# Performance work log

Measured on AMD Instinct MI355X. Metric: run time of the kernel, lower is better.

Reference implementation:

```python
import jax, jax.numpy as jnp
import numpy as np

D_MODEL = 1024
N_HEADS = 16
DH = D_MODEL // N_HEADS
ROPE_THETA = 10000.0


def rotate_half(u):
    h = u.shape[-1] // 2
    return jnp.concatenate([-u[..., h:], u[..., :h]], axis=-1)


def apply_rope(q, k, cos, sin):
    return q * cos + rotate_half(q) * sin, k * cos + rotate_half(k) * sin


def setup_inputs() -> dict:
    key = jax.random.key(0)
    ks = jax.random.split(key, 6)
    B, S = 2, 2048
    x = jax.random.normal(ks[0], (B, S, D_MODEL), dtype=jnp.float32)
    y = jax.random.normal(ks[1], (B, S, D_MODEL), dtype=jnp.float32)
    wq = 0.01 * jax.random.normal(ks[2], (D_MODEL, D_MODEL), dtype=jnp.float32)
    wk = 0.01 * jax.random.normal(ks[3], (D_MODEL, D_MODEL), dtype=jnp.float32)
    wv = 0.01 * jax.random.normal(ks[4], (D_MODEL, D_MODEL), dtype=jnp.float32)
    wo = 0.01 * jax.random.normal(ks[5], (D_MODEL, D_MODEL), dtype=jnp.float32)
    return {"x": x, "y": y, "wq": wq, "wk": wk, "wv": wv, "wo": wo}


def reference(x, y, wq, wk, wv, wo):
    B, S, D = x.shape
    past_length = 0  # default; kv_cache=None

    Q = x @ wq.T                      # (B,S,D)
    K = y                             # NOTE: K is y un-projected (as in source)
    V = y @ wv.T
    # K1 = x @ wk.T is computed in the source but immediately overwritten
    # by the buggy second apply_rope call -> wk is unused in the output.
    V1 = x @ wo.T

    def heads(t):
        return t.reshape(B, S, N_HEADS, DH).transpose(0, 2, 1, 3)  # (B,H,S,dh)

    q_h, k_h, v_h, v1_h = heads(Q), heads(K), heads(V), heads(V1)

    # RoPE tables (past_length:past_length+S rows of the cache)
    freqs = 1.0 / ROPE_THETA ** (jnp.arange(0, DH, 2, dtype=jnp.float32) / DH)
    emb = jnp.arange(past_length, past_length + S, dtype=jnp.float32)[:, None] * freqs[None, :]
    cos = jnp.concatenate([jnp.cos(emb), jnp.cos(emb)], axis=-1)[None, None]  # (1,1,S,dh)
    sin = jnp.concatenate([jnp.sin(emb), jnp.sin(emb)], axis=-1)[None, None]

    q_h, k_h = apply_rope(q_h, k_h, cos, sin)
    # faithful to source: k1 = rope applied AGAIN to the already-roped k
    _, k1_h = apply_rope(q_h, k_h, cos, sin)

    k_full = jnp.concatenate([k_h, k1_h], axis=2)   # (B,H,2S,dh)
    v_full = jnp.concatenate([v_h, v1_h], axis=2)
    S_full = k_full.shape[2]

    # mask: tril(diagonal=past_length) over (S,S_full), last S cols = eye(S)
    rows = jnp.arange(S)[:, None]
    cols = jnp.arange(S_full)[None, :]
    mask = cols <= rows + past_length
    mask = mask.at[:, -S:].set(jnp.eye(S, dtype=bool))  # (S,S_full)

    scores = jnp.einsum("bhqd,bhkd->bhqk", q_h, k_full) / jnp.sqrt(jnp.asarray(DH, x.dtype))
    scores = jnp.where(mask[None, None], scores, jnp.asarray(-1e30, x.dtype))
    attn = jax.nn.softmax(scores, axis=-1)
    out = jnp.einsum("bhqk,bhkd->bhqd", attn, v_full)
    out = out.transpose(0, 2, 1, 3).reshape(B, S, D)

    k_ret = k_full[:, :, :-S, :]
    return out, k_ret
```

## Files before the change

### kernel.cpp

```cpp
#include <hip/hip_runtime.h>

#define DM 1024
#define NHEADS 16
#define DHEAD 64
#define BB 2
#define SS 2048
#define BH (BB*NHEADS)

typedef __attribute__((ext_vector_type(8))) short short8;
typedef __attribute__((ext_vector_type(4))) float float4v;
typedef unsigned short ushort_t;

#define LN1E4_D32 0.28782313662425572f
#define SM_SCALE  0.18033688011112042f

static __device__ __forceinline__ unsigned short f2bf(float f) {
    union { float f; unsigned u; } v; v.f = f;
    unsigned r = v.u + 0x7fffu + ((v.u >> 16) & 1u);
    return (unsigned short)(r >> 16);
}
static __device__ __forceinline__ float bf2f(unsigned short u) {
    union { float f; unsigned u; } v; v.u = ((unsigned)u) << 16;
    return v.f;
}
static __device__ __forceinline__ unsigned cvtpk_bf16(float lo, float hi) {
    unsigned r;
    asm("v_cvt_pk_bf16_f32 %0, %1, %2" : "=v"(r) : "v"(lo), "v"(hi));
    return r;
}
static __device__ __forceinline__ float ex2(float x) {
    float r;
    asm("v_exp_f32 %0, %1" : "=v"(r) : "v"(x));
    return r;
}

static __device__ __forceinline__ void gload16(const ushort_t* g, ushort_t* l) {
    __builtin_amdgcn_global_load_lds(
        (const __attribute__((address_space(1))) void*)g,
        (__attribute__((address_space(3))) void*)l, 16, 0, 0);
}

__global__ __launch_bounds__(256) void prep_kernel(
        const float* __restrict__ x, const float* __restrict__ y,
        const float* __restrict__ wq, const float* __restrict__ wv,
        const float* __restrict__ wo,
        ushort_t* __restrict__ xb, ushort_t* __restrict__ wqb,
        ushort_t* __restrict__ wvb, ushort_t* __restrict__ wob,
        float* __restrict__ kout, ushort_t* __restrict__ khb,
        ushort_t* __restrict__ yb) {
    if (blockIdx.x < 3584) {
        int C = blockIdx.x * 256 + threadIdx.x;
        int c  = C & 511;
        int tl = C >> 9;
        int rb = tl >> 5, kb = tl & 31;
        const float* src; ushort_t* dst; int r0;
        if (rb < 32)      { src = x;  r0 = rb * 128;        dst = xb  + (size_t)tl * 4096; }
        else if (rb < 40) { src = wq; r0 = (rb - 32) * 128; dst = wqb + (size_t)(((rb - 32) * 32) + kb) * 4096; }
        else if (rb < 48) { src = wv; r0 = (rb - 40) * 128; dst = wvb + (size_t)(((rb - 40) * 32) + kb) * 4096; }
        else              { src = wo; r0 = (rb - 48) * 128; dst = wob + (size_t)(((rb - 48) * 32) + kb) * 4096; }
        int row = c >> 2, g = c & 3;
        int kk3 = g ^ ((row >> 1) & 3);
        const float* s = src + (size_t)(r0 + row) * DM + kb * 32 + kk3 * 8;
        float4 a0 = *reinterpret_cast<const float4*>(s);
        float4 a1 = *reinterpret_cast<const float4*>(s + 4);
        short8 v;
        v[0] = (short)f2bf(a0.x); v[1] = (short)f2bf(a0.y);
        v[2] = (short)f2bf(a0.z); v[3] = (short)f2bf(a0.w);
        v[4] = (short)f2bf(a1.x); v[5] = (short)f2bf(a1.y);
        v[6] = (short)f2bf(a1.z); v[7] = (short)f2bf(a1.w);
        *reinterpret_cast<short8*>(dst + c * 8) = v;
        return;
    }
    int t = (blockIdx.x - 3584) * 256 + threadIdx.x;
    int i8 = t & 3;
    int s  = (t >> 2) & (SS - 1);
    int bh = t >> 13;
    int h = bh & (NHEADS - 1), b = bh >> 4;

    const float* yp = y + ((size_t)(b * SS + s)) * DM + h * DHEAD + i8 * 8;
    float4 a0 = *reinterpret_cast<const float4*>(yp);
    float4 a1 = *reinterpret_cast<const float4*>(yp + 4);
    float4 b0 = *reinterpret_cast<const float4*>(yp + 32);
    float4 b1 = *reinterpret_cast<const float4*>(yp + 36);
    float u0[8] = {a0.x, a0.y, a0.z, a0.w, a1.x, a1.y, a1.z, a1.w};
    float u1[8] = {b0.x, b0.y, b0.z, b0.w, b1.x, b1.y, b1.z, b1.w};
    float lo[8], hi[8];
#pragma unroll
    for (int j = 0; j < 8; j++) {
        int i = i8 * 8 + j;
        float freq = __expf(-(float)i * LN1E4_D32);
        float th = (float)s * freq;
        float cv, sv;
        __sincosf(th, &sv, &cv);
        lo[j] = u0[j] * cv - u1[j] * sv;
        hi[j] = u1[j] * cv + u0[j] * sv;
    }
    float* op = kout + ((size_t)bh * SS + s) * DHEAD + i8 * 8;
    *reinterpret_cast<float4*>(op)      = (float4){lo[0], lo[1], lo[2], lo[3]};
    *reinterpret_cast<float4*>(op + 4)  = (float4){lo[4], lo[5], lo[6], lo[7]};
    *reinterpret_cast<float4*>(op + 32) = (float4){hi[0], hi[1], hi[2], hi[3]};
    *reinterpret_cast<float4*>(op + 36) = (float4){hi[4], hi[5], hi[6], hi[7]};

    ushort_t* kb = khb + ((size_t)bh * 32 + (s >> 6)) * 4096 + (s & 63) * 64;
    short8 vlo, vhi;
#pragma unroll
    for (int j = 0; j < 8; j++) { vlo[j] = (short)f2bf(lo[j]); vhi[j] = (short)f2bf(hi[j]); }
    *reinterpret_cast<short8*>(kb + ((i8 ^ (s & 7)) << 3))       = vlo;
    *reinterpret_cast<short8*>(kb + (((i8 + 4) ^ (s & 7)) << 3)) = vhi;

    int rowm = b * SS + s;
    int rowin = rowm & 127, rbm = rowm >> 7;
    int g = i8 ^ ((rowin >> 1) & 3);
    ushort_t* yt = yb + ((size_t)(rbm * 32 + h * 2)) * 4096 + rowin * 32 + (g << 3);
    short8 ulo, uhi;
#pragma unroll
    for (int j = 0; j < 8; j++) { ulo[j] = (short)f2bf(u0[j]); uhi[j] = (short)f2bf(u1[j]); }
    *reinterpret_cast<short8*>(yt)        = ulo;
    *reinterpret_cast<short8*>(yt + 4096) = uhi;
}

__global__ __launch_bounds__(256, 2) void gemm3_kernel(
        const ushort_t* __restrict__ xb, const ushort_t* __restrict__ yb,
        const ushort_t* __restrict__ wqb, const ushort_t* __restrict__ wvb,
        const ushort_t* __restrict__ wob,
        ushort_t* __restrict__ qh, ushort_t* __restrict__ vt, ushort_t* __restrict__ v1h) {
    __shared__ __align__(16) char smem[49152];
    ushort_t* As = (ushort_t*)smem;
    ushort_t* Bs = (ushort_t*)(smem + 16384);
    ushort_t* Cs = (ushort_t*)(smem + 32768);
    ushort_t (*Ct)[136] = (ushort_t(*)[136])smem;

    int bid = blockIdx.x;
    int xcd = bid & 7;
    int s_  = bid >> 3;
    int merged = (s_ < 32);
    int t_  = s_ & 31;
    int n0  = (t_ >> 2) * 128;
    int m0  = (xcd * 4 + (t_ & 3)) * 128;

    const ushort_t* A  = merged ? xb : yb;
    const ushort_t* W1 = merged ? wqb : wvb;

    const ushort_t* Atl = A   + (size_t)(m0 >> 7) * 32 * 4096;
    const ushort_t* W1t = W1  + (size_t)(n0 >> 7) * 32 * 4096;
    const ushort_t* W2t = wob + (size_t)(n0 >> 7) * 32 * 4096;

    int tid = threadIdx.x;
    int wave = tid >> 6, lane = tid & 63, quad = lane >> 4, l15 = lane & 15;
    int wr = (wave >> 1) * 64, wc = (wave & 1) * 64;

    int gi0 = tid * 8, gi1 = (256 + tid) * 8;
    int li0 = (tid & 192) * 8, li1 = (256 + (tid & 192)) * 8;

    int aoff[4], boff[4];
#pragma unroll
    for (int mi = 0; mi < 4; mi++) {
        int row = wr + mi * 16 + l15;
        aoff[mi] = row * 32 + ((quad ^ ((row >> 1) & 3)) << 3);
    }
#pragma unroll
    for (int ni = 0; ni < 4; ni++) {
        int row = wc + ni * 16 + l15;
        boff[ni] = row * 32 + ((quad ^ ((row >> 1) & 3)) << 3);
    }

    float4v acc1[4][4], acc2[4][4];
#pragma unroll
    for (int a = 0; a < 4; a++)
#pragma unroll
        for (int b = 0; b < 4; b++) {
            acc1[a][b] = (float4v){0.f, 0.f, 0.f, 0.f};
            acc2[a][b] = (float4v){0.f, 0.f, 0.f, 0.f};
        }

    gload16(Atl + gi0, As + li0); gload16(Atl + gi1, As + li1);
    gload16(W1t + gi0, Bs + li0); gload16(W1t + gi1, Bs + li1);
    if (merged) { gload16(W2t + gi0, Cs + li0); gload16(W2t + gi1, Cs + li1); }
    int cur = 0;

    for (int kb = 0; kb < 32; kb++) {
        __syncthreads();
        if (kb + 1 < 32) {
            const ushort_t* at = Atl + (size_t)(kb + 1) * 4096;
            const ushort_t* w1 = W1t + (size_t)(kb + 1) * 4096;
            int nb = (cur ^ 1) * 4096;
            gload16(at + gi0, As + nb + li0); gload16(at + gi1, As + nb + li1);
            gload16(w1 + gi0, Bs + nb + li0); gload16(w1 + gi1, Bs + nb + li1);
            if (merged) {
                const ushort_t* w2 = W2t + (size_t)(kb + 1) * 4096;
                gload16(w2 + gi0, Cs + nb + li0); gload16(w2 + gi1, Cs + nb + li1);
            }
        }
        const ushort_t* Ac = As + cur * 4096;
        const ushort_t* Bc = Bs + cur * 4096;
        const ushort_t* Cc = Cs + cur * 4096;
        short8 af[4], b1[4];
#pragma unroll
        for (int mi = 0; mi < 4; mi++)
            af[mi] = *reinterpret_cast<const short8*>(&Ac[aoff[mi]]);
#pragma unroll
        for (int ni = 0; ni < 4; ni++)
            b1[ni] = *reinterpret_cast<const short8*>(&Bc[boff[ni]]);
#pragma unroll
        for (int mi = 0; mi < 4; mi++)
#pragma unroll
            for (int ni = 0; ni < 4; ni++)
                acc1[mi][ni] = __builtin_amdgcn_mfma_f32_16x16x32_bf16(af[mi], b1[ni], acc1[mi][ni], 0, 0, 0);
        if (merged) {
            short8 b2[4];
#pragma unroll
            for (int ni = 0; ni < 4; ni++)
                b2[ni] = *reinterpret_cast<const short8*>(&Cc[boff[ni]]);
#pragma unroll
            for (int mi = 0; mi < 4; mi++)
#pragma unroll
                for (int ni = 0; ni < 4; ni++)
                    acc2[mi][ni] = __builtin_amdgcn_mfma_f32_16x16x32_bf16(af[mi], b2[ni], acc2[mi][ni], 0, 0, 0);
        }
        cur ^= 1;
    }

    int h0 = n0 >> 6;
    if (merged) {
#pragma unroll
        for (int mi = 0; mi < 4; mi++)
#pragma unroll
            for (int r = 0; r < 4; r++) {
                int m = m0 + wr + mi * 16 + quad * 4 + r;
                float pos = (float)(m & (SS - 1));
#pragma unroll
                for (int ni = 0; ni < 2; ni++) {
                    int d = ni * 16 + l15;
                    float f = __expf(-(float)d * LN1E4_D32);
                    float th = pos * f;
                    float cv, sv;
                    __sincosf(th, &sv, &cv);
                    cv *= SM_SCALE; sv *= SM_SCALE;
                    float u0 = acc1[mi][ni][r], u1 = acc1[mi][ni + 2][r];
                    acc1[mi][ni][r]     = u0 * cv - u1 * sv;
                    acc1[mi][ni + 2][r] = u1 * cv + u0 * sv;
                }
            }
        __syncthreads();
#pragma unroll
        for (int mi = 0; mi < 4; mi++)
#pragma unroll
            for (int ni = 0; ni < 4; ni++) {
                int col = wc + ni * 16 + l15;
#pragma unroll
                for (int r = 0; r < 4; r++)
                    Ct[wr + mi * 16 + quad * 4 + r][col] = f2bf(acc1[mi][ni][r]);
            }
        __syncthreads();
#pragma unroll
        for (int it = 0; it < 8; it++) {
            int c = it * 256 + tid;
            int o = c >> 3, j = c & 7;
            int hh = o >> 7, mr = o & 127;
            int m = m0 + mr, b = m >> 11, si = m & (SS - 1);
            uint4 v = *reinterpret_cast<const uint4*>(&Ct[mr][hh * 64 + j * 8]);
            *reinterpret_cast<uint4*>(
                &qh[((size_t)((b * NHEADS + h0 + hh) * SS + si)) * DHEAD + j * 8]) = v;
        }
        __syncthreads();
#pragma unroll
        for (int mi = 0; mi < 4; mi++)
#pragma unroll
            for (int ni = 0; ni < 4; ni++) {
                int col = wc + ni * 16 + l15;
#pragma unroll
                for (int r = 0; r < 4; r++)
                    Ct[wr + mi * 16 + quad * 4 + r][col] = f2bf(acc2[mi][ni][r]);
            }
        __syncthreads();
#pragma unroll
        for (int it = 0; it < 8; it++) {
            int c = it * 256 + tid;
            int o = c >> 3, j = c & 7;
            int hh = o >> 7, mr = o & 127;
            int m = m0 + mr, b = m >> 11, si = m & (SS - 1);
            uint4 v = *reinterpret_cast<const uint4*>(&Ct[mr][hh * 64 + j * 8]);
            *reinterpret_cast<uint4*>(
                &v1h[((size_t)((b * NHEADS + h0 + hh) * SS + si)) * DHEAD + j * 8]) = v;
        }
    } else {
        __syncthreads();
#pragma unroll
        for (int mi = 0; mi < 4; mi++)
#pragma unroll
            for (int ni = 0; ni < 4; ni++) {
                int col = wc + ni * 16 + l15;
#pragma unroll
                for (int r = 0; r < 4; r++)
                    Ct[wr + mi * 16 + quad * 4 + r][col] = f2bf(acc1[mi][ni][r]);
            }
        __syncthreads();
        int b = m0 >> 11;
        int s0 = m0 & (SS - 1);
#pragma unroll
        for (int it = 0; it < 8; it++) {
            int c = it * 256 + tid;
            int dh  = c & 63;
            int k16 = (c >> 6) & 15;
            int hh  = c >> 10;
            short8 v;
#pragma unroll
            for (int e = 0; e < 8; e++)
                v[e] = (short)Ct[k16 * 8 + e][hh * 64 + dh];
            int kt = (s0 >> 6) + (k16 >> 3);
            size_t off = ((size_t)((b * NHEADS + h0 + hh) * 32 + kt)) * 4096
                       + dh * 64 + (((k16 & 7) ^ (dh & 7)) << 3);
            *reinterpret_cast<short8*>(&vt[off]) = v;
        }
    }
}

template<bool MASKED>
static __device__ __forceinline__ void attn_tile(
        const ushort_t* __restrict__ Kc, const ushort_t* __restrict__ Vc, int kbase,
        int quad, int l15, int q0w, const short8* qf, const short8& onesf,
        ushort_t* __restrict__ Psw, float4v* Oa, float4v& sum4) {
    float4v sa[4];
#pragma unroll
    for (int t2 = 0; t2 < 4; t2++) sa[t2] = (float4v){0.f, 0.f, 0.f, 0.f};
    __builtin_amdgcn_s_setprio(1);
#pragma unroll
    for (int t2 = 0; t2 < 4; t2++) {
        int key = t2 * 16 + l15;
        int ro = key * 64, sw = key & 7;
#pragma unroll
        for (int half = 0; half < 2; half++) {
            short8 kf = *reinterpret_cast<const short8*>(&Kc[ro + (((half * 4 + quad) ^ sw) << 3)]);
            sa[t2] = __builtin_amdgcn_mfma_f32_16x16x32_bf16(kf, qf[half], sa[t2], 0, 0, 0);
        }
    }
    __builtin_amdgcn_s_setprio(0);
    int query = q0w + l15;
    int swl = l15 & 7;
#pragma unroll
    for (int t2 = 0; t2 < 4; t2++) {
        float p[4];
#pragma unroll
        for (int r = 0; r < 4; r++) {
            float e = ex2(sa[t2][r]);
            if (MASKED) {
                int key = kbase + t2 * 16 + quad * 4 + r;
                p[r] = (key <= query) ? e : 0.f;
            } else {
                p[r] = e;
            }
        }
        unsigned w0 = cvtpk_bf16(p[0], p[1]);
        unsigned w1 = cvtpk_bf16(p[2], p[3]);
        int chunk = (((t2 * 2 + (quad >> 1)) ^ swl) << 3) + (quad & 1) * 4;
        *reinterpret_cast<unsigned*>(&Psw[l15 * 64 + chunk])     = w0;
        *reinterpret_cast<unsigned*>(&Psw[l15 * 64 + chunk + 2]) = w1;
    }
    short8 pf0 = *reinterpret_cast<const short8*>(&Psw[l15 * 64 + ((quad ^ swl) << 3)]);
    short8 pf1 = *reinterpret_cast<const short8*>(&Psw[l15 * 64 + (((4 + quad) ^ swl) << 3)]);
    __builtin_amdgcn_s_setprio(1);
#pragma unroll
    for (int t = 0; t < 4; t++) {
        int dh = t * 16 + l15;
        int ro = dh * 64, sw = dh & 7;
        short8 vf0 = *reinterpret_cast<const short8*>(&Vc[ro + ((quad ^ sw) << 3)]);
        short8 vf1 = *reinterpret_cast<const short8*>(&Vc[ro + (((4 + quad) ^ sw) << 3)]);
        Oa[t] = __builtin_amdgcn_mfma_f32_16x16x32_bf16(pf0, vf0, Oa[t], 0, 0, 0);
        Oa[t] = __builtin_amdgcn_mfma_f32_16x16x32_bf16(pf1, vf1, Oa[t], 0, 0, 0);
    }
    sum4 = __builtin_amdgcn_mfma_f32_16x16x32_bf16(pf0, onesf, sum4, 0, 0, 0);
    sum4 = __builtin_amdgcn_mfma_f32_16x16x32_bf16(pf1, onesf, sum4, 0, 0, 0);
    __builtin_amdgcn_s_setprio(0);
}

__global__ __launch_bounds__(512, 4) void attn_kernel(
        const ushort_t* __restrict__ qh, const float* __restrict__ kf32,
        const ushort_t* __restrict__ khb, const ushort_t* __restrict__ vtb,
        const ushort_t* __restrict__ v1h, float* __restrict__ out) {
    __shared__ __align__(16) ushort_t Ks[4][4096];
    __shared__ __align__(16) ushort_t Vt[4][4096];
    __shared__ __align__(16) ushort_t Ps[8][1024];

    int bid = blockIdx.x;
    int bh = (bid & 7) * 4 + ((bid >> 3) & 3);
    int p  = bid >> 5;

    int tid = threadIdx.x, wave = tid >> 6, lane = tid & 63, quad = lane >> 4, l15 = lane & 15;
    int jq  = (wave < 4) ? p : (31 - p);
    int q0w = jq * 64 + (wave & 3) * 16;
    const ushort_t* qp  = qh  + (size_t)bh * SS * DHEAD;
    const float*    kp  = kf32 + (size_t)bh * SS * DHEAD;
    const ushort_t* v1p = v1h + (size_t)bh * SS * DHEAD;
    const ushort_t* ktb = khb + (size_t)bh * 32 * 4096;
    const ushort_t* vtt = vtb + (size_t)bh * 32 * 4096;

    short8 qf[2];
    qf[0] = *reinterpret_cast<const short8*>(&qp[(q0w + l15) * DHEAD + quad * 8]);
    qf[1] = *reinterpret_cast<const short8*>(&qp[(q0w + l15) * DHEAD + 32 + quad * 8]);
    short8 onesf;
#pragma unroll
    for (int j = 0; j < 8; j++) onesf[j] = (short)0x3F80;

    float4v Oa[4];
#pragma unroll
    for (int t = 0; t < 4; t++) Oa[t] = (float4v){0.f, 0.f, 0.f, 0.f};
    float4v sum4 = (float4v){0.f, 0.f, 0.f, 0.f};

    int gi = tid * 8;
    int li = (tid & 448) * 8;

    int ntiles = 32 - p;
    gload16(ktb + gi, &Ks[0][li]);               gload16(vtt + gi, &Vt[0][li]);
    gload16(ktb + 4096 + gi, &Ks[1][li]);        gload16(vtt + 4096 + gi, &Vt[1][li]);

    int kt = 0;
    for (; kt + 1 < ntiles; kt += 2) {
        __syncthreads();
        if (kt + 2 < ntiles) {
            const ushort_t* gk = ktb + (size_t)(kt + 2) * 4096;
            const ushort_t* gv = vtt + (size_t)(kt + 2) * 4096;
            int nb = (kt + 2) & 3;
            gload16(gk + gi, &Ks[nb][li]);
            gload16(gv + gi, &Vt[nb][li]);
        }
        if (kt + 3 < ntiles) {
            const ushort_t* gk = ktb + (size_t)(kt + 3) * 4096;
            const ushort_t* gv = vtt + (size_t)(kt + 3) * 4096;
            int nb = (kt + 3) & 3;
            gload16(gk + gi, &Ks[nb][li]);
            gload16(gv + gi, &Vt[nb][li]);
        }
        {
            int kbase = kt * 64, sl = kt & 3;
            if (kbase <= q0w + 15) {
                if (kbase + 63 <= q0w)
                    attn_tile<false>(Ks[sl], Vt[sl], kbase, quad, l15, q0w, qf, onesf,
                                     &Ps[wave][0], Oa, sum4);
                else
                    attn_tile<true>(Ks[sl], Vt[sl], kbase, quad, l15, q0w, qf, onesf,
                                    &Ps[wave][0], Oa, sum4);
            }
        }
        {
            int kbase = (kt + 1) * 64, sl = (kt + 1) & 3;
            if (kbase <= q0w + 15) {
                if (kbase + 63 <= q0w)
                    attn_tile<false>(Ks[sl], Vt[sl], kbase, quad, l15, q0w, qf, onesf,
                                     &Ps[wave][0], Oa, sum4);
                else
                    attn_tile<true>(Ks[sl], Vt[sl], kbase, quad, l15, q0w, qf, onesf,
                                    &Ps[wave][0], Oa, sum4);
            }
        }
    }
    if (kt < ntiles) {
        __syncthreads();
        int kbase = kt * 64, sl = kt & 3;
        if (kbase <= q0w + 15) {
            if (kbase + 63 <= q0w)
                attn_tile<false>(Ks[sl], Vt[sl], kbase, quad, l15, q0w, qf, onesf,
                                 &Ps[wave][0], Oa, sum4);
            else
                attn_tile<true>(Ks[sl], Vt[sl], kbase, quad, l15, q0w, qf, onesf,
                                &Ps[wave][0], Oa, sum4);
        }
    }

    float* sdiag = reinterpret_cast<float*>(&Ps[wave][32]);

    {
        int sk = q0w + l15;
        const float* krow = kp + (size_t)sk * DHEAD;
        short8 k1lo, k1hi;
#pragma unroll
        for (int j = 0; j < 8; j++) {
            int d = quad * 8 + j;
            float f = __expf(-(float)d * LN1E4_D32);
            float th = (float)sk * f;
            float cv, sv;
            __sincosf(th, &sv, &cv);
            float a = krow[d], b2 = krow[d + 32];
            k1lo[j] = (short)f2bf(a * cv - b2 * sv);
            k1hi[j] = (short)f2bf(b2 * cv + a * sv);
        }
        float4v sd4 = (float4v){0.f, 0.f, 0.f, 0.f};
        sd4 = __builtin_amdgcn_mfma_f32_16x16x32_bf16(qf[0], k1lo, sd4, 0, 0, 0);
        sd4 = __builtin_amdgcn_mfma_f32_16x16x32_bf16(qf[1], k1hi, sd4, 0, 0, 0);
#pragma unroll
        for (int r = 0; r < 4; r++)
            if (l15 == quad * 4 + r) sdiag[l15] = sd4[r];

        int b = bh >> 4, h = bh & (NHEADS - 1);
#pragma unroll
        for (int r = 0; r < 4; r++) {
            float pd = ex2(sdiag[quad * 4 + r]);
            int query = q0w + quad * 4 + r;
            float linv = 1.f / (sum4[r] + pd);
#pragma unroll
            for (int t = 0; t < 4; t++) {
                float v1v = bf2f(v1p[query * DHEAD + t * 16 + l15]);
                float o = (Oa[t][r] + pd * v1v) * linv;
                out[(b * SS + query) * DM + h * DHEAD + t * 16 + l15] = o;
            }
        }
    }
}

extern "C" void kernel_launch(void* const* d_in, const int* in_sizes, int n_in,
                              void* d_out, int out_size, void* d_ws, size_t ws_size,
                              hipStream_t stream) {
    const float* x  = (const float*)d_in[0];
    const float* y  = (const float*)d_in[1];
    const float* wq = (const float*)d_in[2];
    const float* wv = (const float*)d_in[4];
    const float* wo = (const float*)d_in[5];
    float* outp  = (float*)d_out;
    float* k_out = outp + (size_t)BB * SS * DM;

    char* ws = (char*)d_ws;
    ushort_t* vtb = (ushort_t*)(ws);
    ushort_t* v1b = (ushort_t*)(ws + (8ull  << 20));
    ushort_t* qhb = (ushort_t*)(ws + (16ull << 20));
    ushort_t* khb = (ushort_t*)(ws + (24ull << 20));
    ushort_t* xb  = (ushort_t*)(ws + (32ull << 20));
    ushort_t* yb  = (ushort_t*)(ws + (40ull << 20));
    ushort_t* wqb = (ushort_t*)(ws + (48ull << 20));
    ushort_t* wvb = (ushort_t*)(ws + (50ull << 20));
    ushort_t* wob = (ushort_t*)(ws + (52ull << 20));

    prep_kernel<<<4608, 256, 0, stream>>>(x, y, wq, wv, wo, xb, wqb, wvb, wob,
                                          k_out, khb, yb);
    gemm3_kernel<<<512, 256, 0, stream>>>(xb, yb, wqb, wvb, wob, qhb, vtb, v1b);
    attn_kernel<<<512, 512, 0, stream>>>(qhb, k_out, khb, vtb, v1b, outp);
}
```

Measured before the change: 167.5 us.

## Keep softmax probabilities in registers via 16x16x16 MFMA and reorder V layout

Removes the per-wave LDS round trip for the P matrix. The score accumulator layout is fed directly as the A operand of 16x16x16 bf16 MFMAs. The V-transpose writer in the projection kernel is changed so each lane's 8-element V chunk matches the key ordering the register-resident P fragments use, and the row-sum now uses four small MFMAs against a ones vector. The cost is twice as many (smaller) MFMA instructions in exchange for dropping the LDS stores, loads and the Ps buffer.

```diff
diff --git a/kernel.cpp b/kernel.cpp
--- a/kernel.cpp
+++ b/kernel.cpp
@@ -8,6 +8,7 @@
 #define BH (BB*NHEADS)
 
 typedef __attribute__((ext_vector_type(8))) short short8;
+typedef __attribute__((ext_vector_type(4))) short short4v;
 typedef __attribute__((ext_vector_type(4))) float float4v;
 typedef unsigned short ushort_t;
 
@@ -32,6 +33,12 @@
     float r;
     asm("v_exp_f32 %0, %1" : "=v"(r) : "v"(x));
     return r;
+}
+static __device__ __forceinline__ short4v lo4(short8 v) {
+    return __builtin_shufflevector(v, v, 0, 1, 2, 3);
+}
+static __device__ __forceinline__ short4v hi4(short8 v) {
+    return __builtin_shufflevector(v, v, 4, 5, 6, 7);
 }
 
 static __device__ __forceinline__ void gload16(const ushort_t* g, ushort_t* l) {
@@ -300,16 +307,22 @@
 #pragma unroll
         for (int it = 0; it < 8; it++) {
             int c = it * 256 + tid;
-            int dh  = c & 63;
-            int k16 = (c >> 6) & 15;
-            int hh  = c >> 10;
+            int dh6 = c & 63;
+            int rest = c >> 6;
+            int hh = rest >> 4;
+            int th = (rest >> 3) & 1;
+            int cq = rest & 7;
+            int q = cq >> 1, sHalf = cq & 1;
             short8 v;
 #pragma unroll
-            for (int e = 0; e < 8; e++)
-                v[e] = (short)Ct[k16 * 8 + e][hh * 64 + dh];
-            int kt = (s0 >> 6) + (k16 >> 3);
+            for (int e = 0; e < 8; e++) {
+                int t2 = 2 * sHalf + (e >> 2), j = e & 3;
+                int kw = 16 * t2 + 4 * q + j;
+                v[e] = (short)Ct[th * 64 + kw][hh * 64 + dh6];
+            }
+            int kt = (s0 >> 6) + th;
             size_t off = ((size_t)((b * NHEADS + h0 + hh) * 32 + kt)) * 4096
-                       + dh * 64 + (((k16 & 7) ^ (dh & 7)) << 3);
+                       + dh6 * 64 + ((cq ^ (dh6 & 7)) << 3);
             *reinterpret_cast<short8*>(&vt[off]) = v;
         }
     }
@@ -318,8 +331,8 @@
 template<bool MASKED>
 static __device__ __forceinline__ void attn_tile(
         const ushort_t* __restrict__ Kc, const ushort_t* __restrict__ Vc, int kbase,
-        int quad, int l15, int q0w, const short8* qf, const short8& onesf,
-        ushort_t* __restrict__ Psw, float4v* Oa, float4v& sum4) {
+        int quad, int l15, int q0w, const short8* qf, const short4v& ones4,
+        float4v* Oa, float4v& sum4) {
     float4v sa[4];
 #pragma unroll
     for (int t2 = 0; t2 < 4; t2++) sa[t2] = (float4v){0.f, 0.f, 0.f, 0.f};
@@ -336,7 +349,7 @@
     }
     __builtin_amdgcn_s_setprio(0);
     int query = q0w + l15;
-    int swl = l15 & 7;
+    short4v pa[4];
 #pragma unroll
     for (int t2 = 0; t2 < 4; t2++) {
         float p[4];
@@ -350,26 +363,26 @@
                 p[r] = e;
             }
         }
-        unsigned w0 = cvtpk_bf16(p[0], p[1]);
-        unsigned w1 = cvtpk_bf16(p[2], p[3]);
-        int chunk = (((t2 * 2 + (quad >> 1)) ^ swl) << 3) + (quad & 1) * 4;
-        *reinterpret_cast<unsigned*>(&Psw[l15 * 64 + chunk])     = w0;
-        *reinterpret_cast<unsigned*>(&Psw[l15 * 64 + chunk + 2]) = w1;
-    }
-    short8 pf0 = *reinterpret_cast<const short8*>(&Psw[l15 * 64 + ((quad ^ swl) << 3)]);
-    short8 pf1 = *reinterpret_cast<const short8*>(&Psw[l15 * 64 + (((4 + quad) ^ swl) << 3)]);
+        union { short4v s; unsigned u[2]; } pu;
+        pu.u[0] = cvtpk_bf16(p[0], p[1]);
+        pu.u[1] = cvtpk_bf16(p[2], p[3]);
+        pa[t2] = pu.s;
+    }
     __builtin_amdgcn_s_setprio(1);
+#pragma unroll
+    for (int t2 = 0; t2 < 4; t2++)
+        sum4 = __builtin_amdgcn_mfma_f32_16x16x16bf16_1k(pa[t2], ones4, sum4, 0, 0, 0);
 #pragma unroll
     for (int t = 0; t < 4; t++) {
         int dh = t * 16 + l15;
         int ro = dh * 64, sw = dh & 7;
-        short8 vf0 = *reinterpret_cast<const short8*>(&Vc[ro + ((quad ^ sw) << 3)]);
-        short8 vf1 = *reinterpret_cast<const short8*>(&Vc[ro + (((4 + quad) ^ sw) << 3)]);
-        Oa[t] = __builtin_amdgcn_mfma_f32_16x16x32_bf16(pf0, vf0, Oa[t], 0, 0, 0);
-        Oa[t] = __builtin_amdgcn_mfma_f32_16x16x32_bf16(pf1, vf1, Oa[t], 0, 0, 0);
-    }
-    sum4 = __builtin_amdgcn_mfma_f32_16x16x32_bf16(pf0, onesf, sum4, 0, 0, 0);
-    sum4 = __builtin_amdgcn_mfma_f32_16x16x32_bf16(pf1, onesf, sum4, 0, 0, 0);
+        short8 v0 = *reinterpret_cast<const short8*>(&Vc[ro + (((quad * 2 + 0) ^ sw) << 3)]);
+        short8 v1 = *reinterpret_cast<const short8*>(&Vc[ro + (((quad * 2 + 1) ^ sw) << 3)]);
+        Oa[t] = __builtin_amdgcn_mfma_f32_16x16x16bf16_1k(pa[0], lo4(v0), Oa[t], 0, 0, 0);
+        Oa[t] = __builtin_amdgcn_mfma_f32_16x16x16bf16_1k(pa[1], hi4(v0), Oa[t], 0, 0, 0);
+        Oa[t] = __builtin_amdgcn_mfma_f32_16x16x16bf16_1k(pa[2], lo4(v1), Oa[t], 0, 0, 0);
+        Oa[t] = __builtin_amdgcn_mfma_f32_16x16x16bf16_1k(pa[3], hi4(v1), Oa[t], 0, 0, 0);
+    }
     __builtin_amdgcn_s_setprio(0);
 }
 
@@ -379,7 +392,7 @@
         const ushort_t* __restrict__ v1h, float* __restrict__ out) {
     __shared__ __align__(16) ushort_t Ks[4][4096];
     __shared__ __align__(16) ushort_t Vt[4][4096];
-    __shared__ __align__(16) ushort_t Ps[8][1024];
+    __shared__ float sdiag_s[8][16];
 
     int bid = blockIdx.x;
     int bh = (bid & 7) * 4 + ((bid >> 3) & 3);
@@ -397,9 +410,9 @@
     short8 qf[2];
     qf[0] = *reinterpret_cast<const short8*>(&qp[(q0w + l15) * DHEAD + quad * 8]);
     qf[1] = *reinterpret_cast<const short8*>(&qp[(q0w + l15) * DHEAD + 32 + quad * 8]);
-    short8 onesf;
-#pragma unroll
-    for (int j = 0; j < 8; j++) onesf[j] = (short)0x3F80;
+    short4v ones4;
+#pragma unroll
+    for (int j = 0; j < 4; j++) ones4[j] = (short)0x3F80;
 
     float4v Oa[4];
 #pragma unroll
@@ -434,22 +447,18 @@
             int kbase = kt * 64, sl = kt & 3;
             if (kbase <= q0w + 15) {
                 if (kbase + 63 <= q0w)
-                    attn_tile<false>(Ks[sl], Vt[sl], kbase, quad, l15, q0w, qf, onesf,
-                                     &Ps[wave][0], Oa, sum4);
+                    attn_tile<false>(Ks[sl], Vt[sl], kbase, quad, l15, q0w, qf, ones4, Oa, sum4);
                 else
-                    attn_tile<true>(Ks[sl], Vt[sl], kbase, quad, l15, q0w, qf, onesf,
-                                    &Ps[wave][0], Oa, sum4);
+                    attn_tile<true>(Ks[sl], Vt[sl], kbase, quad, l15, q0w, qf, ones4, Oa, sum4);
             }
         }
         {
             int kbase = (kt + 1) * 64, sl = (kt + 1) & 3;
             if (kbase <= q0w + 15) {
                 if (kbase + 63 <= q0w)
-                    attn_tile<false>(Ks[sl], Vt[sl], kbase, quad, l15, q0w, qf, onesf,
-                                     &Ps[wave][0], Oa, sum4);
+                    attn_tile<false>(Ks[sl], Vt[sl], kbase, quad, l15, q0w, qf, ones4, Oa, sum4);
                 else
-                    attn_tile<true>(Ks[sl], Vt[sl], kbase, quad, l15, q0w, qf, onesf,
-                                    &Ps[wave][0], Oa, sum4);
+                    attn_tile<true>(Ks[sl], Vt[sl], kbase, quad, l15, q0w, qf, ones4, Oa, sum4);
             }
         }
     }
@@ -458,15 +467,13 @@
         int kbase = kt * 64, sl = kt & 3;
         if (kbase <= q0w + 15) {
             if (kbase + 63 <= q0w)
-                attn_tile<false>(Ks[sl], Vt[sl], kbase, quad, l15, q0w, qf, onesf,
-                                 &Ps[wave][0], Oa, sum4);
+                attn_tile<false>(Ks[sl], Vt[sl], kbase, quad, l15, q0w, qf, ones4, Oa, sum4);
             else
-                attn_tile<true>(Ks[sl], Vt[sl], kbase, quad, l15, q0w, qf, onesf,
-                                &Ps[wave][0], Oa, sum4);
-        }
-    }
-
-    float* sdiag = reinterpret_cast<float*>(&Ps[wave][32]);
+                attn_tile<true>(Ks[sl], Vt[sl], kbase, quad, l15, q0w, qf, ones4, Oa, sum4);
+        }
+    }
+
+    float* sdiag = sdiag_s[wave];
 
     {
         int sk = q0w + l15;
```

New measurement: 164.3 us. No clear change (-1.9%).
